# Performance work log

Hardware: AMD Instinct MI355X
Metric: run time of the kernel (lower is better)

## Reference

```python
import jax, jax.numpy as jnp
import numpy as np

B, S, D, H = 2, 2048, 1024, 16
MASK_VAL = -50000.0

def setup_inputs() -> dict:
    key = jax.random.key(0)
    k1, k2, k3, k4 = jax.random.split(key, 4)
    # weights stored as [in, out] so projection is x @ W (equals torch Linear with W.T)
    s = 1.0 / np.sqrt(D)
    return {
        "x": jax.random.normal(k1, (B, S, D), dtype=jnp.float32),
        "Wq": jax.random.normal(k2, (D, D), dtype=jnp.float32) * s,
        "Wkv": jax.random.normal(k3, (D, 2 * D), dtype=jnp.float32) * s,
        "Wo": jax.random.normal(k4, (D, D), dtype=jnp.float32) * s,
    }

def reference(x, Wq, Wkv, Wo):
    b, sl, d = x.shape
    h = H
    hd = d // h
    scale = hd ** (-0.5)
    q = x @ Wq                      # [b, sl, d]
    kv = x @ Wkv                    # [b, sl, 2d]
    k, v = jnp.split(kv, 2, axis=-1)
    # [b, h, s, hd]
    q = q.reshape(b, sl, h, hd).transpose(0, 2, 1, 3)
    k = k.reshape(b, sl, h, hd).transpose(0, 2, 1, 3)
    v = v.reshape(b, sl, h, hd).transpose(0, 2, 1, 3)
    dots = jnp.einsum('bhid,bhjd->bhij', q * scale, k)  # [b,h,s,s]
    # causal: strictly-upper-triangular entries set to MASK_VAL
    causal = jnp.tril(jnp.ones((sl, sl), dtype=bool))
    dots = jnp.where(causal, dots, MASK_VAL)
    attn = jax.nn.softmax(dots, axis=-1)
    out = jnp.einsum('bhij,bhjd->bihd', attn, v).reshape(b, sl, d)
    return out @ Wo
```

## Files before the change

kernel.cpp:

```cpp
#include <hip/hip_runtime.h>

typedef __bf16 bf16_t;
typedef unsigned short u16;
typedef __attribute__((ext_vector_type(8))) __bf16 bf16x8;
typedef __attribute__((ext_vector_type(4))) float f32x4;
typedef __attribute__((ext_vector_type(4))) u16 u16x4;
typedef __attribute__((ext_vector_type(8))) u16 u16x8;

#define SS 2048

__device__ __forceinline__ u16 f2b(float f) {
    return __builtin_bit_cast(u16, (__bf16)f);
}

__device__ __forceinline__ float fexp2(float x) {
#if __has_builtin(__builtin_amdgcn_exp2f)
    return __builtin_amdgcn_exp2f(x);
#else
    float r;
    asm("v_exp_f32 %0, %1" : "=v"(r) : "v"(x));
    return r;
#endif
}

__device__ __forceinline__ void async_copy16(const u16* g, u16* l) {
    __builtin_amdgcn_global_load_lds(
        (__attribute__((address_space(1))) void*)(u16*)g,
        (__attribute__((address_space(3))) void*)l, 16, 0, 0);
}

__device__ __forceinline__ bf16x8 ldfrag(const u16* p) {
    return __builtin_bit_cast(bf16x8, *(const u16x8*)p);
}

__global__ __launch_bounds__(256)
void cast_x_kernel(const float* __restrict__ x, u16* __restrict__ xb) {
    size_t i = ((size_t)blockIdx.x * 256 + threadIdx.x) * 8;
    float4 a = *(const float4*)(x + i);
    float4 b = *(const float4*)(x + i + 4);
    u16x8 o;
    o[0] = f2b(a.x); o[1] = f2b(a.y); o[2] = f2b(a.z); o[3] = f2b(a.w);
    o[4] = f2b(b.x); o[5] = f2b(b.y); o[6] = f2b(b.z); o[7] = f2b(b.w);
    *(u16x8*)(xb + i) = o;
}

__global__ __launch_bounds__(256)
void transpose_all(const float* __restrict__ Wq, const float* __restrict__ Wkv,
                   const float* __restrict__ Wo, u16* __restrict__ WcatT,
                   u16* __restrict__ WoT) {
    const int z = blockIdx.z;
    if (z != 1 && blockIdx.y >= 16) return;
    const float* src; u16* dst; int N; float scale;
    if (z == 0)      { src = Wq;  dst = WcatT;               N = 1024; scale = 0.125f * 1.44269504089f; }
    else if (z == 1) { src = Wkv; dst = WcatT + 1024 * 1024; N = 2048; scale = 1.0f; }
    else             { src = Wo;  dst = WoT;                 N = 1024; scale = 1.0f; }
    __shared__ __attribute__((aligned(16))) u16 tile[64][72];
    const int k0 = blockIdx.x * 64, n0 = blockIdx.y * 64;
    const int tid = threadIdx.x;
#pragma unroll
    for (int p = 0; p < 4; ++p) {
        int c = p * 256 + tid;
        int r = c >> 4, c4 = c & 15;
        float4 v = *(const float4*)(src + (size_t)(k0 + r) * N + n0 + c4 * 4);
        u16x4 o;
        o[0] = f2b(v.x * scale); o[1] = f2b(v.y * scale);
        o[2] = f2b(v.z * scale); o[3] = f2b(v.w * scale);
        *(u16x4*)&tile[r][c4 * 4] = o;
    }
    __syncthreads();
#pragma unroll
    for (int p = 0; p < 4; ++p) {
        int c = p * 256 + tid;
        int n = c >> 4, k4 = c & 15;
        u16x4 o;
#pragma unroll
        for (int i = 0; i < 4; ++i) o[i] = tile[k4 * 4 + i][n];
        *(u16x4*)(dst + (size_t)(n0 + n) * 1024 + k0 + k4 * 4) = o;
    }
}

template <typename OutT>
__global__ __launch_bounds__(256, 3)
void gemm_bt(const u16* __restrict__ A, const u16* __restrict__ BT,
             OutT* __restrict__ C, u16* __restrict__ VTg, int M, int N, int K) {
    __shared__ __attribute__((aligned(16))) u16 As[2][128 * 32];
    __shared__ __attribute__((aligned(16))) u16 Bs[2][128 * 32];
    const int tid = threadIdx.x;
    const int wave = tid >> 6, lane = tid & 63;
    const int l15 = lane & 15, quad = lane >> 4;
    const int wid = blockIdx.x;
    const int per = (int)(gridDim.x >> 3);
    const int logical = (wid & 7) * per + (wid >> 3);
    const int nxt = N >> 7;
    const int ty = logical / nxt, tx = logical - ty * nxt;
    const int m0 = ty * 128, n0 = tx * 128;
    const int wm = (wave >> 1) * 64, wn = (wave & 1) * 64;
    const f32x4 zero = {0.f, 0.f, 0.f, 0.f};
    f32x4 acc[4][4];
#pragma unroll
    for (int i = 0; i < 4; ++i)
#pragma unroll
        for (int j = 0; j < 4; ++j) acc[i][j] = zero;
    const int r0 = tid >> 2, kc = (tid & 3) * 8;
    auto stage = [&](int bsel, int k0) {
        async_copy16(A + (size_t)(m0 + r0) * K + k0 + kc, As[bsel] + tid * 8);
        async_copy16(BT + (size_t)(n0 + r0) * K + k0 + kc, Bs[bsel] + tid * 8);
        async_copy16(A + (size_t)(m0 + 64 + r0) * K + k0 + kc, As[bsel] + (256 + tid) * 8);
        async_copy16(BT + (size_t)(n0 + 64 + r0) * K + k0 + kc, Bs[bsel] + (256 + tid) * 8);
    };
    stage(0, 0);
    __syncthreads();
    const int nk = K >> 5;
    for (int t = 0; t < nk; ++t) {
        if (t + 1 < nk) stage((t + 1) & 1, (t + 1) * 32);
        const u16* Ab = As[t & 1];
        const u16* Bb = Bs[t & 1];
        bf16x8 af[4], bf[4];
#pragma unroll
        for (int s = 0; s < 4; ++s) {
            af[s] = ldfrag(Ab + (wm + s * 16 + l15) * 32 + quad * 8);
            bf[s] = ldfrag(Bb + (wn + s * 16 + l15) * 32 + quad * 8);
        }
#pragma unroll
        for (int mt = 0; mt < 4; ++mt)
#pragma unroll
            for (int nt = 0; nt < 4; ++nt)
                acc[mt][nt] = __builtin_amdgcn_mfma_f32_16x16x32_bf16(
                    af[mt], bf[nt], acc[mt][nt], 0, 0, 0);
        __syncthreads();
    }
    if constexpr (sizeof(OutT) == 2) {
        if (n0 >= 2048) {
#pragma unroll
            for (int mt = 0; mt < 4; ++mt)
#pragma unroll
                for (int nt = 0; nt < 4; ++nt) {
                    const int n_g = n0 + wn + nt * 16 + l15 - 2048;
                    const int hd = n_g & 63, h = n_g >> 6;
                    const int m_g = m0 + wm + mt * 16 + quad * 4;
                    const int bb = m_g >> 11;
                    const int s = m_g & 2047;
                    const int sb = s & 63;
                    const int col = (sb & 32) | ((sb & 12) << 1) | ((sb >> 2) & 4);
                    u16x4 o;
#pragma unroll
                    for (int r = 0; r < 4; ++r) o[r] = f2b(acc[mt][nt][r]);
                    *(u16x4*)(VTg + ((size_t)(bb * 16 + h) * 64 + hd) * 2048
                              + (s & ~63) + col) = o;
                }
            return;
        }
    }
#pragma unroll
    for (int mt = 0; mt < 4; ++mt)
#pragma unroll
        for (int nt = 0; nt < 4; ++nt) {
            const int n = n0 + wn + nt * 16 + l15;
#pragma unroll
            for (int r = 0; r < 4; ++r) {
                const int m = m0 + wm + mt * 16 + quad * 4 + r;
                float v = acc[mt][nt][r];
                if constexpr (sizeof(OutT) == 2) C[(size_t)m * N + n] = (OutT)f2b(v);
                else                             C[(size_t)m * N + n] = v;
            }
        }
}

__global__ __launch_bounds__(256, 2)
void gemm_bt64(const u16* __restrict__ A, const u16* __restrict__ BT,
               float* __restrict__ C, int M, int N, int K) {
    __shared__ __attribute__((aligned(16))) u16 As[2][128 * 32];
    __shared__ __attribute__((aligned(16))) u16 Bs[2][64 * 32];
    const int tid = threadIdx.x;
    const int wave = tid >> 6, lane = tid & 63;
    const int l15 = lane & 15, quad = lane >> 4;
    const int wid = blockIdx.x;
    const int per = (int)(gridDim.x >> 3);
    const int logical = (wid & 7) * per + (wid >> 3);
    const int nxt = N >> 6;
    const int ty = logical / nxt, tx = logical - ty * nxt;
    const int m0 = ty * 128, n0 = tx * 64;
    const int wm = (wave >> 1) * 64, wn = (wave & 1) * 32;
    const f32x4 zero = {0.f, 0.f, 0.f, 0.f};
    f32x4 acc[4][2];
#pragma unroll
    for (int i = 0; i < 4; ++i)
#pragma unroll
        for (int j = 0; j < 2; ++j) acc[i][j] = zero;
    const int r0 = tid >> 2, kc = (tid & 3) * 8;
    auto stage = [&](int bsel, int k0) {
        async_copy16(A + (size_t)(m0 + r0) * K + k0 + kc, As[bsel] + tid * 8);
        async_copy16(A + (size_t)(m0 + 64 + r0) * K + k0 + kc, As[bsel] + (256 + tid) * 8);
        async_copy16(BT + (size_t)(n0 + r0) * K + k0 + kc, Bs[bsel] + tid * 8);
    };
    stage(0, 0);
    __syncthreads();
    const int nk = K >> 5;
    for (int t = 0; t < nk; ++t) {
        if (t + 1 < nk) stage((t + 1) & 1, (t + 1) * 32);
        const u16* Ab = As[t & 1];
        const u16* Bb = Bs[t & 1];
        bf16x8 af[4], bf[2];
#pragma unroll
        for (int s = 0; s < 4; ++s)
            af[s] = ldfrag(Ab + (wm + s * 16 + l15) * 32 + quad * 8);
#pragma unroll
        for (int s = 0; s < 2; ++s)
            bf[s] = ldfrag(Bb + (wn + s * 16 + l15) * 32 + quad * 8);
#pragma unroll
        for (int mt = 0; mt < 4; ++mt)
#pragma unroll
            for (int nt = 0; nt < 2; ++nt)
                acc[mt][nt] = __builtin_amdgcn_mfma_f32_16x16x32_bf16(
                    af[mt], bf[nt], acc[mt][nt], 0, 0, 0);
        __syncthreads();
    }
#pragma unroll
    for (int mt = 0; mt < 4; ++mt)
#pragma unroll
        for (int nt = 0; nt < 2; ++nt) {
            const int n = n0 + wn + nt * 16 + l15;
#pragma unroll
            for (int r = 0; r < 4; ++r) {
                const int m = m0 + wm + mt * 16 + quad * 4 + r;
                C[(size_t)m * N + n] = acc[mt][nt][r];
            }
        }
}

__global__ __launch_bounds__(256, 2)
void attn_kernel(const u16* __restrict__ QKV, const u16* __restrict__ VTg,
                 u16* __restrict__ AO) {
    __shared__ __attribute__((aligned(16))) u16 Kt[2][2 * 64 * 32];
    __shared__ __attribute__((aligned(16))) u16 Vt[2][2 * 64 * 32];
    const int tid = threadIdx.x;
    const int wave = tid >> 6, lane = tid & 63;
    const int l15 = lane & 15, quad = lane >> 4;
    const int w16 = wave * 16;
    const int wid = blockIdx.x;
    const int g = wid >> 3;
    const int jj = g & 15, hf = jj >> 1;
    const int xe0 = (jj & 1) ? 15 - hf : hf;
    const int xe = (g & 32) ? 15 - xe0 : xe0;
    const int bh = (wid & 7) * 4 + (g >> 4);
    const int b = bh >> 4, h = bh & 15;
    const int qbA = 31 - xe, qbB = xe;
    const int qA0 = qbA * 64, qB0 = qbB * 64;
    const size_t bS = (size_t)b * SS;
    const u16* vbase = VTg + (size_t)bh * 64 * 2048;
    const int rr = (tid >> 2) & 63, kc8 = (tid & 3) * 8;

    {
        const u16* ksrc = QKV + (bS + rr) * 3072 + 1024 + h * 64 + kc8;
        async_copy16(ksrc,      Kt[0] + tid * 8);
        async_copy16(ksrc + 32, Kt[0] + (256 + tid) * 8);
        const u16* vsrc = vbase + (size_t)rr * 2048 + kc8;
        async_copy16(vsrc,      Vt[0] + tid * 8);
        async_copy16(vsrc + 32, Vt[0] + (256 + tid) * 8);
    }
    bf16x8 qfA[2], qfB[2];
    {
        const u16* qA = QKV + (bS + qA0 + w16 + l15) * 3072 + h * 64 + quad * 8;
        qfA[0] = ldfrag(qA); qfA[1] = ldfrag(qA + 32);
        const u16* qB = QKV + (bS + qB0 + w16 + l15) * 3072 + h * 64 + quad * 8;
        qfB[0] = ldfrag(qB); qfB[1] = ldfrag(qB + 32);
    }
    float lA = 0.f, lB = 0.f;
    f32x4 OA[4], OB[4];
    const f32x4 zero = {0.f, 0.f, 0.f, 0.f};
#pragma unroll
    for (int nt = 0; nt < 4; ++nt) { OA[nt] = zero; OB[nt] = zero; }
    const f32x4 cinit = {-10.f, -10.f, -10.f, -10.f};
    __syncthreads();

    for (int j = 0; j <= qbA; ++j) {
        if (j < qbA) {
            const int kv1 = (j + 1) * 64;
            const int nb = (j + 1) & 1;
            const u16* ksrc = QKV + (bS + kv1 + rr) * 3072 + 1024 + h * 64 + kc8;
            async_copy16(ksrc,      Kt[nb] + tid * 8);
            async_copy16(ksrc + 32, Kt[nb] + (256 + tid) * 8);
            const u16* vsrc = vbase + (size_t)rr * 2048 + kv1 + kc8;
            async_copy16(vsrc,      Vt[nb] + tid * 8);
            async_copy16(vsrc + 32, Vt[nb] + (256 + tid) * 8);
        }
        const bool bAct = (j <= qbB);
        const bool dA = (j == qbA), dB = (j == qbB);
        const u16* KB = Kt[j & 1];
        const u16* VB = Vt[j & 1];
        bf16x8 vf[4][2];
#pragma unroll
        for (int nt = 0; nt < 4; ++nt)
#pragma unroll
            for (int ks = 0; ks < 2; ++ks)
                vf[nt][ks] = ldfrag(VB + ks * 2048 + (nt * 16 + l15) * 32 + quad * 8);
        u16x4 pcA[4], pcB[4];
#pragma unroll
        for (int c = 0; c < 4; ++c) {
            bf16x8 kf0 = ldfrag(KB + (c * 16 + l15) * 32 + quad * 8);
            bf16x8 kf1 = ldfrag(KB + 2048 + (c * 16 + l15) * 32 + quad * 8);
            f32x4 a = __builtin_amdgcn_mfma_f32_16x16x32_bf16(kf0, qfA[0], cinit, 0, 0, 0);
            f32x4 s = __builtin_amdgcn_mfma_f32_16x16x32_bf16(kf1, qfA[1], a, 0, 0, 0);
            if (dA) {
#pragma unroll
                for (int r = 0; r < 4; ++r)
                    if (c * 16 + quad * 4 + r > w16 + l15) s[r] = -1e30f;
            }
            u16x4 pk; float acc = 0.f;
#pragma unroll
            for (int r = 0; r < 4; ++r) {
                float pv = fexp2(s[r]);
                acc += pv;
                pk[r] = f2b(pv);
            }
            lA += acc; pcA[c] = pk;
            if (bAct) {
                f32x4 a2 = __builtin_amdgcn_mfma_f32_16x16x32_bf16(kf0, qfB[0], cinit, 0, 0, 0);
                f32x4 s2 = __builtin_amdgcn_mfma_f32_16x16x32_bf16(kf1, qfB[1], a2, 0, 0, 0);
                if (dB) {
#pragma unroll
                    for (int r = 0; r < 4; ++r)
                        if (c * 16 + quad * 4 + r > w16 + l15) s2[r] = -1e30f;
                }
                u16x4 pk2; float acc2 = 0.f;
#pragma unroll
                for (int r = 0; r < 4; ++r) {
                    float pv = fexp2(s2[r]);
                    acc2 += pv;
                    pk2[r] = f2b(pv);
                }
                lB += acc2; pcB[c] = pk2;
            }
        }
        bf16x8 paA[2], paB[2];
#pragma unroll
        for (int ks = 0; ks < 2; ++ks) {
            u16x8 t;
#pragma unroll
            for (int i = 0; i < 4; ++i) { t[i] = pcA[2 * ks][i]; t[4 + i] = pcA[2 * ks + 1][i]; }
            paA[ks] = __builtin_bit_cast(bf16x8, t);
        }
#pragma unroll
        for (int nt = 0; nt < 4; ++nt) {
            OA[nt] = __builtin_amdgcn_mfma_f32_16x16x32_bf16(paA[0], vf[nt][0], OA[nt], 0, 0, 0);
            OA[nt] = __builtin_amdgcn_mfma_f32_16x16x32_bf16(paA[1], vf[nt][1], OA[nt], 0, 0, 0);
        }
        if (bAct) {
#pragma unroll
            for (int ks = 0; ks < 2; ++ks) {
                u16x8 t;
#pragma unroll
                for (int i = 0; i < 4; ++i) { t[i] = pcB[2 * ks][i]; t[4 + i] = pcB[2 * ks + 1][i]; }
                paB[ks] = __builtin_bit_cast(bf16x8, t);
            }
#pragma unroll
            for (int nt = 0; nt < 4; ++nt) {
                OB[nt] = __builtin_amdgcn_mfma_f32_16x16x32_bf16(paB[0], vf[nt][0], OB[nt], 0, 0, 0);
                OB[nt] = __builtin_amdgcn_mfma_f32_16x16x32_bf16(paB[1], vf[nt][1], OB[nt], 0, 0, 0);
            }
        }
        __syncthreads();
    }

    lA += __shfl_xor(lA, 16); lA += __shfl_xor(lA, 32);
    lB += __shfl_xor(lB, 16); lB += __shfl_xor(lB, 32);
#pragma unroll
    for (int r = 0; r < 4; ++r) {
        const int ql = quad * 4 + r;
        float invA = 1.0f / __shfl(lA, ql);
        float invB = 1.0f / __shfl(lB, ql);
        size_t rowA = bS + (size_t)qA0 + w16 + ql;
        size_t rowB = bS + (size_t)qB0 + w16 + ql;
#pragma unroll
        for (int nt = 0; nt < 4; ++nt) {
            AO[rowA * 1024 + h * 64 + nt * 16 + l15] = f2b(OA[nt][r] * invA);
            AO[rowB * 1024 + h * 64 + nt * 16 + l15] = f2b(OB[nt][r] * invB);
        }
    }
}

extern "C" void kernel_launch(void* const* d_in, const int* in_sizes, int n_in,
                              void* d_out, int out_size, void* d_ws, size_t ws_size,
                              hipStream_t stream) {
    (void)in_sizes; (void)n_in; (void)out_size; (void)ws_size;
    const float* x   = (const float*)d_in[0];
    const float* Wq  = (const float*)d_in[1];
    const float* Wkv = (const float*)d_in[2];
    const float* Wo  = (const float*)d_in[3];
    float* out = (float*)d_out;
    char* ws = (char*)d_ws;
    u16* xb    = (u16*)(ws);
    u16* WcatT = (u16*)(ws + (size_t)(8 << 20));
    u16* WoT   = (u16*)(ws + (size_t)(14 << 20));
    u16* QKV   = (u16*)(ws + (size_t)(16 << 20));
    u16* VTb   = (u16*)(ws + (size_t)(40 << 20));
    u16* AO    = xb;

    cast_x_kernel<<<2048, 256, 0, stream>>>(x, xb);
    transpose_all<<<dim3(16, 32, 3), 256, 0, stream>>>(Wq, Wkv, Wo, WcatT, WoT);
    gemm_bt<u16><<<768, 256, 0, stream>>>(xb, WcatT, QKV, VTb, 4096, 3072, 1024);
    attn_kernel<<<512, 256, 0, stream>>>(QKV, VTb, AO);
    gemm_bt64<<<512, 256, 0, stream>>>(AO, WoT, out, 4096, 1024, 1024);
}
```

Baseline: 170.4 us.

## Rewrite QKV GEMM as 256x256-tile 8-wave kernel with phased async pipeline

Replaces the 128x128-tile, 4-wave QKV projection GEMM with a 256x256-tile, 512-thread kernel that uses 64-wide K stages and XOR-swizzled LDS layouts. Global-to-LDS copies are split into eight phases interleaved with MFMA work, using explicit vmcnt waits, barriers and setprio. The aim is higher arithmetic intensity per tile and better overlap of memory with compute. In exchange it uses more LDS and registers per block and launches only 192 blocks, so fewer blocks fit per CU and the GPU may be poorly filled.

After: 179.8 us. 5.5% more time.

```diff
diff --git a/kernel.cpp b/kernel.cpp
--- a/kernel.cpp
+++ b/kernel.cpp
@@ -79,90 +79,136 @@
     }
 }
 
-template <typename OutT>
-__global__ __launch_bounds__(256, 3)
-void gemm_bt(const u16* __restrict__ A, const u16* __restrict__ BT,
-             OutT* __restrict__ C, u16* __restrict__ VTg, int M, int N, int K) {
-    __shared__ __attribute__((aligned(16))) u16 As[2][128 * 32];
-    __shared__ __attribute__((aligned(16))) u16 Bs[2][128 * 32];
+__global__ __launch_bounds__(512, 2)
+void gemm_qkv8(const u16* __restrict__ A, const u16* __restrict__ BT,
+               u16* __restrict__ C, u16* __restrict__ VTg) {
+    constexpr int K = 1024;
+    constexpr int NITER = 8;
+    __shared__ __attribute__((aligned(16))) u16 As[2][16384];
+    __shared__ __attribute__((aligned(16))) u16 Bs[2][16384];
     const int tid = threadIdx.x;
     const int wave = tid >> 6, lane = tid & 63;
     const int l15 = lane & 15, quad = lane >> 4;
+    const int wm = wave >> 2, wn = wave & 3;
     const int wid = blockIdx.x;
-    const int per = (int)(gridDim.x >> 3);
-    const int logical = (wid & 7) * per + (wid >> 3);
-    const int nxt = N >> 7;
-    const int ty = logical / nxt, tx = logical - ty * nxt;
-    const int m0 = ty * 128, n0 = tx * 128;
-    const int wm = (wave >> 1) * 64, wn = (wave & 1) * 64;
+    const int logical = (wid & 7) * 24 + (wid >> 3);
+    const int ty = logical / 12, tx = logical - ty * 12;
+    const int m0 = ty * 256, n0 = tx * 256;
+    const int r0h = tid >> 3, c0 = (tid & 7) * 8;
+    const int csrc = c0 ^ (((r0h >> 2) & 1) << 4);
+    const int cq = (quad * 8) ^ (((l15 >> 2) & 1) << 4);
+
+    f32x4 acc[8][4];
     const f32x4 zero = {0.f, 0.f, 0.f, 0.f};
-    f32x4 acc[4][4];
-#pragma unroll
-    for (int i = 0; i < 4; ++i)
+#pragma unroll
+    for (int i = 0; i < 8; ++i)
 #pragma unroll
         for (int j = 0; j < 4; ++j) acc[i][j] = zero;
-    const int r0 = tid >> 2, kc = (tid & 3) * 8;
-    auto stage = [&](int bsel, int k0) {
-        async_copy16(A + (size_t)(m0 + r0) * K + k0 + kc, As[bsel] + tid * 8);
-        async_copy16(BT + (size_t)(n0 + r0) * K + k0 + kc, Bs[bsel] + tid * 8);
-        async_copy16(A + (size_t)(m0 + 64 + r0) * K + k0 + kc, As[bsel] + (256 + tid) * 8);
-        async_copy16(BT + (size_t)(n0 + 64 + r0) * K + k0 + kc, Bs[bsel] + (256 + tid) * 8);
+
+    auto stageA = [&](int buf, int half, int kt) {
+        const u16* s = A + (size_t)(m0 + half * 128 + r0h) * K + kt * 64 + csrc;
+        u16* d = &As[buf][half * 8192 + tid * 8];
+        async_copy16(s, d);
+        async_copy16(s + (size_t)64 * K, d + 4096);
     };
-    stage(0, 0);
-    __syncthreads();
-    const int nk = K >> 5;
-    for (int t = 0; t < nk; ++t) {
-        if (t + 1 < nk) stage((t + 1) & 1, (t + 1) * 32);
-        const u16* Ab = As[t & 1];
-        const u16* Bb = Bs[t & 1];
-        bf16x8 af[4], bf[4];
-#pragma unroll
-        for (int s = 0; s < 4; ++s) {
-            af[s] = ldfrag(Ab + (wm + s * 16 + l15) * 32 + quad * 8);
-            bf[s] = ldfrag(Bb + (wn + s * 16 + l15) * 32 + quad * 8);
-        }
-#pragma unroll
-        for (int mt = 0; mt < 4; ++mt)
-#pragma unroll
-            for (int nt = 0; nt < 4; ++nt)
-                acc[mt][nt] = __builtin_amdgcn_mfma_f32_16x16x32_bf16(
-                    af[mt], bf[nt], acc[mt][nt], 0, 0, 0);
-        __syncthreads();
-    }
-    if constexpr (sizeof(OutT) == 2) {
-        if (n0 >= 2048) {
-#pragma unroll
-            for (int mt = 0; mt < 4; ++mt)
-#pragma unroll
-                for (int nt = 0; nt < 4; ++nt) {
-                    const int n_g = n0 + wn + nt * 16 + l15 - 2048;
-                    const int hd = n_g & 63, h = n_g >> 6;
-                    const int m_g = m0 + wm + mt * 16 + quad * 4;
-                    const int bb = m_g >> 11;
-                    const int s = m_g & 2047;
-                    const int sb = s & 63;
-                    const int col = (sb & 32) | ((sb & 12) << 1) | ((sb >> 2) & 4);
-                    u16x4 o;
-#pragma unroll
-                    for (int r = 0; r < 4; ++r) o[r] = f2b(acc[mt][nt][r]);
-                    *(u16x4*)(VTg + ((size_t)(bb * 16 + h) * 64 + hd) * 2048
-                              + (s & ~63) + col) = o;
+    auto stageB = [&](int buf, int half, int kt) {
+        const u16* s = BT + (size_t)(n0 + half * 128 + r0h) * K + kt * 64 + csrc;
+        u16* d = &Bs[buf][half * 8192 + tid * 8];
+        async_copy16(s, d);
+        async_copy16(s + (size_t)64 * K, d + 4096);
+    };
+    auto dsA = [&](int buf, int mf, int ks) {
+        return ldfrag(&As[buf][wm * 8192 + (mf * 16 + l15) * 64 + ks * 32 + cq]);
+    };
+    auto dsB = [&](int buf, int nf, int ks) {
+        return ldfrag(&Bs[buf][(wn >> 1) * 8192 +
+                               ((wn & 1) * 64 + nf * 16 + l15) * 64 + ks * 32 + cq]);
+    };
+
+    stageA(0, 0, 0); stageA(0, 1, 0);
+    stageB(0, 0, 0); stageB(0, 1, 0);
+    stageB(1, 0, 1); stageB(1, 1, 1);
+    asm volatile("s_waitcnt vmcnt(4)" ::: "memory");
+    __builtin_amdgcn_s_barrier();
+
+    for (int i = 0; i < NITER; ++i) {
+        const bool lastI = (i == NITER - 1);
+        const int t1 = 2 * i + 1, t2 = 2 * i + 2, t3 = 2 * i + 3;
+        bf16x8 bf[4][2], af[2][2];
+#pragma unroll
+        for (int ph = 0; ph < 8; ++ph) {
+            const int kb = ph >> 2;
+            const int q = ph & 3;
+            af[0][0] = dsA(kb, q * 2, 0);     af[0][1] = dsA(kb, q * 2, 1);
+            af[1][0] = dsA(kb, q * 2 + 1, 0); af[1][1] = dsA(kb, q * 2 + 1, 1);
+            if (q == 0) {
+#pragma unroll
+                for (int nf = 0; nf < 4; ++nf) {
+                    bf[nf][0] = dsB(kb, nf, 0);
+                    bf[nf][1] = dsB(kb, nf, 1);
                 }
-            return;
-        }
-    }
-#pragma unroll
-    for (int mt = 0; mt < 4; ++mt)
-#pragma unroll
-        for (int nt = 0; nt < 4; ++nt) {
-            const int n = n0 + wn + nt * 16 + l15;
-#pragma unroll
-            for (int r = 0; r < 4; ++r) {
-                const int m = m0 + wm + mt * 16 + quad * 4 + r;
-                float v = acc[mt][nt][r];
-                if constexpr (sizeof(OutT) == 2) C[(size_t)m * N + n] = (OutT)f2b(v);
-                else                             C[(size_t)m * N + n] = v;
-            }
+            }
+            if (ph == 0)      stageA(1, 0, t1);
+            else if (ph == 1) stageA(1, 1, t1);
+            else if (!lastI) {
+                if (ph == 2)      stageB(0, 0, t2);
+                else if (ph == 3) stageB(0, 1, t2);
+                else if (ph == 4) stageA(0, 0, t2);
+                else if (ph == 5) stageA(0, 1, t2);
+                else if (ph == 6) stageB(1, 0, t3);
+                else              stageB(1, 1, t3);
+            }
+            __builtin_amdgcn_s_barrier();
+            __builtin_amdgcn_s_setprio(1);
+#pragma unroll
+            for (int mfq = 0; mfq < 2; ++mfq)
+#pragma unroll
+                for (int nf = 0; nf < 4; ++nf) {
+                    acc[q * 2 + mfq][nf] = __builtin_amdgcn_mfma_f32_16x16x32_bf16(
+                        af[mfq][0], bf[nf][0], acc[q * 2 + mfq][nf], 0, 0, 0);
+                    acc[q * 2 + mfq][nf] = __builtin_amdgcn_mfma_f32_16x16x32_bf16(
+                        af[mfq][1], bf[nf][1], acc[q * 2 + mfq][nf], 0, 0, 0);
+                }
+            __builtin_amdgcn_s_setprio(0);
+            if (ph == 3) {
+                if (lastI) asm volatile("s_waitcnt vmcnt(0)" ::: "memory");
+                else       asm volatile("s_waitcnt vmcnt(4)" ::: "memory");
+            } else if (ph == 7 && !lastI) {
+                asm volatile("s_waitcnt vmcnt(4)" ::: "memory");
+            }
+            __builtin_amdgcn_s_barrier();
+        }
+    }
+
+    if (n0 >= 2048) {
+#pragma unroll
+        for (int mf = 0; mf < 8; ++mf)
+#pragma unroll
+            for (int nf = 0; nf < 4; ++nf) {
+                const int n_g = n0 + wn * 64 + nf * 16 + l15 - 2048;
+                const int hd = n_g & 63, h = n_g >> 6;
+                const int m_g = m0 + wm * 128 + mf * 16 + quad * 4;
+                const int bb = m_g >> 11;
+                const int s = m_g & 2047;
+                const int sb = s & 63;
+                const int col = (sb & 32) | ((sb & 12) << 1) | ((sb >> 2) & 4);
+                u16x4 o;
+#pragma unroll
+                for (int r = 0; r < 4; ++r) o[r] = f2b(acc[mf][nf][r]);
+                *(u16x4*)(VTg + ((size_t)(bb * 16 + h) * 64 + hd) * 2048
+                          + (s & ~63) + col) = o;
+            }
+        return;
+    }
+#pragma unroll
+    for (int mf = 0; mf < 8; ++mf)
+#pragma unroll
+        for (int nf = 0; nf < 4; ++nf) {
+            const int n = n0 + wn * 64 + nf * 16 + l15;
+            const int mb = m0 + wm * 128 + mf * 16 + quad * 4;
+#pragma unroll
+            for (int r = 0; r < 4; ++r)
+                C[(size_t)(mb + r) * 3072 + n] = f2b(acc[mf][nf][r]);
         }
 }
 
@@ -398,7 +444,7 @@
 
     cast_x_kernel<<<2048, 256, 0, stream>>>(x, xb);
     transpose_all<<<dim3(16, 32, 3), 256, 0, stream>>>(Wq, Wkv, Wo, WcatT, WoT);
-    gemm_bt<u16><<<768, 256, 0, stream>>>(xb, WcatT, QKV, VTb, 4096, 3072, 1024);
+    gemm_qkv8<<<192, 512, 0, stream>>>(xb, WcatT, QKV, VTb);
     attn_kernel<<<512, 256, 0, stream>>>(QKV, VTb, AO);
     gemm_bt64<<<512, 256, 0, stream>>>(AO, WoT, out, 4096, 1024, 1024);
 }
```
